# Performance work log

Hardware: AMD Instinct MI355X
Metric: run time of the kernel (lower is better)

The kernel has to match this reference:

```python
import jax, jax.numpy as jnp
import numpy as np

B, N, R = 4, 16, 64        # batch, permuted axis size, inner spatial size
M, S = N // 2, R * 2       # block count, block size


def _glorot(key, shape):
    fan_in, fan_out = shape[-2], shape[-1]
    lim = np.sqrt(6.0 / (fan_in + fan_out)).astype(np.float32)
    return jax.random.uniform(key, shape, jnp.float32, -lim, lim)


def setup_inputs() -> dict:
    key = jax.random.key(0)
    ks = jax.random.split(key, 10)
    inp = {
        "x": jax.random.normal(ks[0], (B, N, R, N, R, 2), jnp.float32),
        "perm_idx": jax.random.permutation(ks[1], N).astype(jnp.int32),
    }
    for i, name in enumerate(["hr1", "hi1", "hr2", "hi2", "hr3", "hi3", "hr4", "hi4"]):
        inp[name] = _glorot(ks[2 + i], (M, S, S))
    return inp


def _bilin(v, p_right, p_left):
    # v: (B, m, s, m, s). First contract the last s-axis against p_right's
    # block matmuls (block index = axis 3), then the axis-2 s-axis against
    # p_left's block matmuls (block index = axis 1).
    t = jnp.einsum('bmiaj,ajk->bmiak', v, p_right)
    return jnp.einsum('xbjci,bjk->xbkci', t, p_left)


def reference(x, perm_idx, hr1, hi1, hr2, hi2, hr3, hi3, hr4, hi4):
    m = x.shape[1] // 2
    s = x.shape[2] * 2
    n, r = m * 2, s // 2
    x = x.take(perm_idx, axis=1).take(perm_idx, axis=3)
    x = x.reshape((-1, m, s, m, s, 2))
    x_re, x_im = x[..., 0], x[..., 1]

    y_re = (_bilin(x_re, hr1, hr1) + _bilin(x_re, hi1, hi1)
            + _bilin(x_im, hi2, hr2) + _bilin(x_im, hr2, hi2))
    y_im = (_bilin(x_im, hr3, hr3) + _bilin(x_im, hi3, hi3)
            + _bilin(x_re, hi4, hr4) + _bilin(x_re, hr4, hi4))

    y = jnp.stack([y_re, y_im], axis=-1)
    return y.reshape((-1, n, r, n, r, 2))
```

## Files before the change

kernel.cpp:

```cpp
#include <hip/hip_runtime.h>
#include <hip/hip_bf16.h>
#include <stdint.h>

typedef __attribute__((ext_vector_type(8))) short bf16x8;
typedef __attribute__((ext_vector_type(4))) float f32x4;
typedef __attribute__((ext_vector_type(16))) float f32x16;

#define MFMA32(a, b, c) __builtin_amdgcn_mfma_f32_32x32x16_bf16((a), (b), (c), 0, 0, 0)

__device__ __forceinline__ unsigned short f2bf_rn(float f) {
    union { __bf16 b; unsigned short u; } v;
    v.b = (__bf16)f;
    return v.u;
}

__device__ __forceinline__ unsigned int pk2(float lo, float hi) {
    union { unsigned short s[2]; unsigned int u; } r;
    r.s[0] = f2bf_rn(lo); r.s[1] = f2bf_rn(hi);
    return r.u;
}

__device__ __forceinline__ void gload_lds16(const void* g, void* l) {
    __builtin_amdgcn_global_load_lds(
        (const __attribute__((address_space(1))) void*)g,
        (__attribute__((address_space(3))) void*)l, 16, 0, 0);
}

__global__ __launch_bounds__(256) void prep_h(
    const float* __restrict__ h0, const float* __restrict__ h1,
    const float* __restrict__ h2, const float* __restrict__ h3,
    const float* __restrict__ h4, const float* __restrict__ h5,
    const float* __restrict__ h6, const float* __restrict__ h7,
    unsigned short* __restrict__ ht)
{
    const float* hmap[8] = {h0, h1, h2, h3, h4, h5, h6, h7};
    const int wg = blockIdx.x;
    const int jblk = wg >> 2, qt = wg & 3;
    const float* src = hmap[jblk >> 3] + (jblk & 7) * 16384;
    unsigned short* dst = ht + jblk * 16384;
    __shared__ unsigned short tile[32 * 129];
    const int t = threadIdx.x;
    #pragma unroll
    for (int i = 0; i < 16; ++i) {
        int idx = t + 256 * i;
        int r = idx >> 5, kk = idx & 31;
        tile[kk * 129 + r] = f2bf_rn(src[r * 128 + qt * 32 + kk]);
    }
    __syncthreads();
    #pragma unroll
    for (int i = 0; i < 16; ++i) {
        int idx = t + 256 * i;
        int k = idx >> 7, r = idx & 127;
        dst[(qt * 32 + k) * 128 + r] = tile[k * 129 + r];
    }
}

__global__ __launch_bounds__(256, 1) void bilin_main(
    const float* __restrict__ x, const int* __restrict__ perm,
    const unsigned short* __restrict__ ht, float* __restrict__ out)
{
    const int wg = blockIdx.x;
    const int q = wg & 7, p = (wg >> 3) & 7, b = wg >> 6;
    const int tid = threadIdx.x;
    const int lane = tid & 63, wn = tid >> 6;
    const int l31 = lane & 31, hl = lane >> 5;

    __shared__ __align__(16) unsigned short smem[81920];
    unsigned short* xre_lds = smem;
    unsigned short* xim_lds = smem + 16384;
    unsigned short* llds = smem + 65536;

    constexpr int cseq[8]  = {0, 1, 6, 7, 2, 3, 4, 5};
    constexpr int rperm[8] = {0, 1, 3, 2, 4, 5, 7, 6};

    const int wubase = tid & ~63;
    auto stage_h = [&](unsigned short* dst, int blk) {
        const unsigned short* src = ht + blk * 16384;
        #pragma unroll
        for (int r = 0; r < 8; ++r) {
            const int idx = r * 256 + tid;
            const int row = idx >> 4, cin = idx & 15;
            gload_lds16(src + row * 128 + ((cin ^ (row & 15)) << 3),
                        dst + ((r * 256 + wubase) << 3));
        }
    };

    auto ldr = [&](const unsigned short* base, int row, int ch) -> bf16x8 {
        return *(const bf16x8*)(base + row * 128 + ((ch ^ (row & 15)) << 3));
    };

    auto stage_x_both = [&]() {
        #pragma unroll
        for (int i = 0; i < 8; ++i) {
            const int idx = i * 256 + tid;
            const int row = idx >> 4, cin = idx & 15;
            const int n1 = perm[2 * p + (row >> 6)];
            const int n2 = perm[2 * q + (cin >> 3)];
            const int r1 = row & 63, r2 = (cin & 7) * 8;
            const float* sp = x + ((size_t)((b * 16 + n1) * 64 + r1) * 1024
                                   + n2 * 64 + r2) * 2;
            float4 v0 = *(const float4*)(sp);
            float4 v1 = *(const float4*)(sp + 4);
            float4 v2 = *(const float4*)(sp + 8);
            float4 v3 = *(const float4*)(sp + 12);
            bf16x8 re, im;
            re[0] = (short)f2bf_rn(v0.x); re[1] = (short)f2bf_rn(v0.z);
            re[2] = (short)f2bf_rn(v1.x); re[3] = (short)f2bf_rn(v1.z);
            re[4] = (short)f2bf_rn(v2.x); re[5] = (short)f2bf_rn(v2.z);
            re[6] = (short)f2bf_rn(v3.x); re[7] = (short)f2bf_rn(v3.z);
            im[0] = (short)f2bf_rn(v0.y); im[1] = (short)f2bf_rn(v0.w);
            im[2] = (short)f2bf_rn(v1.y); im[3] = (short)f2bf_rn(v1.w);
            im[4] = (short)f2bf_rn(v2.y); im[5] = (short)f2bf_rn(v2.w);
            im[6] = (short)f2bf_rn(v3.y); im[7] = (short)f2bf_rn(v3.w);
            const int woff = row * 128 + ((cin ^ (row & 15)) << 3);
            *(bf16x8*)(xre_lds + woff) = re;
            *(bf16x8*)(xim_lds + woff) = im;
        }
    };

    bf16x8 xf[4][8];
    auto load_xf = [&](const unsigned short* plane) {
        #pragma unroll
        for (int m2 = 0; m2 < 4; ++m2)
            #pragma unroll
            for (int ks = 0; ks < 8; ++ks)
                xf[m2][ks] = ldr(plane, m2 * 32 + l31, 2 * ks + hl);
    };

    stage_h(smem + 32768, rperm[0] * 8 + q);
    stage_h(llds, 0 * 8 + p);
    stage_x_both();
    __syncthreads();
    load_xf(xre_lds);

    f32x16 yre[4], yim[4];
    #pragma unroll
    for (int i = 0; i < 4; ++i) {
        #pragma unroll
        for (int e = 0; e < 16; ++e) { yre[i][e] = 0.f; yim[i][e] = 0.f; }
    }

    #pragma unroll
    for (int cc = 0; cc < 8; ++cc) {
        const unsigned short* wb = smem + 32768 + (cc & 1) * 16384;

        if (cc < 7)
            stage_h(smem + 32768 + ((cc + 1) & 1) * 16384,
                    rperm[cseq[cc + 1]] * 8 + q);

        if (cc == 4) load_xf(xim_lds);

        f32x16 u[4];
        #pragma unroll
        for (int m2 = 0; m2 < 4; ++m2)
            #pragma unroll
            for (int e = 0; e < 16; ++e) u[m2][e] = 0.f;
        #pragma unroll
        for (int ks = 0; ks < 8; ++ks) {
            bf16x8 wfr = ldr(wb, wn * 32 + l31, 2 * ks + hl);
            #pragma unroll
            for (int m2 = 0; m2 < 4; ++m2)
                u[m2] = MFMA32(xf[m2][ks], wfr, u[m2]);
        }

        __syncthreads();

        #pragma unroll
        for (int t = 0; t < 8; ++t) {
            const int f = t >> 1, qa = (t & 1) * 2, qb = qa + 1;
            unsigned int lo0 = pk2(u[f][4 * qa + 0], u[f][4 * qa + 1]);
            unsigned int lo1 = pk2(u[f][4 * qa + 2], u[f][4 * qa + 3]);
            unsigned int hi0 = pk2(u[f][4 * qb + 0], u[f][4 * qb + 1]);
            unsigned int hi1 = pk2(u[f][4 * qb + 2], u[f][4 * qb + 3]);
            unsigned int send0 = hl ? lo0 : hi0;
            unsigned int send1 = hl ? lo1 : hi1;
            unsigned int sx0 = (unsigned int)__shfl_xor((int)send0, 32);
            unsigned int sx1 = (unsigned int)__shfl_xor((int)send1, 32);
            union { unsigned int d[4]; bf16x8 v; } ufu;
            ufu.d[0] = hl ? sx0 : lo0;
            ufu.d[1] = hl ? sx1 : lo1;
            ufu.d[2] = hl ? hi0 : sx0;
            ufu.d[3] = hl ? hi1 : sx1;
            #pragma unroll
            for (int mt = 0; mt < 4; ++mt) {
                bf16x8 lfr = ldr(llds, mt * 32 + l31, 2 * t + hl);
                if ((cc & 3) < 2) yre[mt] = MFMA32(lfr, ufu.v, yre[mt]);
                else              yim[mt] = MFMA32(lfr, ufu.v, yim[mt]);
            }
        }

        __syncthreads();
        if (cc < 7)
            stage_h(llds, cseq[cc + 1] * 8 + p);
    }

    float2* o2 = (float2*)out;
    #pragma unroll
    for (int mt = 0; mt < 4; ++mt)
        #pragma unroll
        for (int j = 0; j < 16; ++j) {
            const int row = mt * 32 + (j & 3) + 8 * (j >> 2) + 4 * hl;
            float2 v;
            v.x = yre[mt][j];
            v.y = yim[mt][j];
            o2[(size_t)(b * 1024 + p * 128 + row) * 1024
               + q * 128 + wn * 32 + l31] = v;
        }
}

extern "C" void kernel_launch(void* const* d_in, const int* in_sizes, int n_in,
                              void* d_out, int out_size, void* d_ws, size_t ws_size,
                              hipStream_t stream) {
    const float* x  = (const float*)d_in[0];
    const int* perm = (const int*)d_in[1];
    unsigned short* htp = (unsigned short*)d_ws;

    hipLaunchKernelGGL(prep_h, dim3(256), dim3(256), 0, stream,
        (const float*)d_in[2], (const float*)d_in[3], (const float*)d_in[4],
        (const float*)d_in[5], (const float*)d_in[6], (const float*)d_in[7],
        (const float*)d_in[8], (const float*)d_in[9], htp);
    hipLaunchKernelGGL(bilin_main, dim3(256), dim3(256), 0, stream,
        x, perm, htp, (float*)d_out);
}
```

Before: 39.48 us.

## Software-pipeline first and second block matmuls with double-buffered left weights

Restructures the main loop so the first-stage GEMM for the next chunk is interleaved with the second-stage GEMM of the current chunk. The right weights become triple-staged and the left weights double-buffered, which removes one barrier per iteration. Only one x plane is kept in LDS and it is restaged from global memory for the imaginary half. The goal is to hide LDS staging latency and keep the MFMA units busy, at the cost of higher register pressure and a second global read of x.

```diff
diff --git a/kernel.cpp b/kernel.cpp
--- a/kernel.cpp
+++ b/kernel.cpp
@@ -66,9 +66,7 @@
     const int l31 = lane & 31, hl = lane >> 5;
 
     __shared__ __align__(16) unsigned short smem[81920];
-    unsigned short* xre_lds = smem;
-    unsigned short* xim_lds = smem + 16384;
-    unsigned short* llds = smem + 65536;
+    unsigned short* xplane = smem;
 
     constexpr int cseq[8]  = {0, 1, 6, 7, 2, 3, 4, 5};
     constexpr int rperm[8] = {0, 1, 3, 2, 4, 5, 7, 6};
@@ -89,7 +87,7 @@
         return *(const bf16x8*)(base + row * 128 + ((ch ^ (row & 15)) << 3));
     };
 
-    auto stage_x_both = [&]() {
+    auto stage_x = [&](int g) {
         #pragma unroll
         for (int i = 0; i < 8; ++i) {
             const int idx = i * 256 + tid;
@@ -103,54 +101,47 @@
             float4 v1 = *(const float4*)(sp + 4);
             float4 v2 = *(const float4*)(sp + 8);
             float4 v3 = *(const float4*)(sp + 12);
-            bf16x8 re, im;
-            re[0] = (short)f2bf_rn(v0.x); re[1] = (short)f2bf_rn(v0.z);
-            re[2] = (short)f2bf_rn(v1.x); re[3] = (short)f2bf_rn(v1.z);
-            re[4] = (short)f2bf_rn(v2.x); re[5] = (short)f2bf_rn(v2.z);
-            re[6] = (short)f2bf_rn(v3.x); re[7] = (short)f2bf_rn(v3.z);
-            im[0] = (short)f2bf_rn(v0.y); im[1] = (short)f2bf_rn(v0.w);
-            im[2] = (short)f2bf_rn(v1.y); im[3] = (short)f2bf_rn(v1.w);
-            im[4] = (short)f2bf_rn(v2.y); im[5] = (short)f2bf_rn(v2.w);
-            im[6] = (short)f2bf_rn(v3.y); im[7] = (short)f2bf_rn(v3.w);
-            const int woff = row * 128 + ((cin ^ (row & 15)) << 3);
-            *(bf16x8*)(xre_lds + woff) = re;
-            *(bf16x8*)(xim_lds + woff) = im;
+            bf16x8 t;
+            if (g == 0) {
+                t[0] = (short)f2bf_rn(v0.x); t[1] = (short)f2bf_rn(v0.z);
+                t[2] = (short)f2bf_rn(v1.x); t[3] = (short)f2bf_rn(v1.z);
+                t[4] = (short)f2bf_rn(v2.x); t[5] = (short)f2bf_rn(v2.z);
+                t[6] = (short)f2bf_rn(v3.x); t[7] = (short)f2bf_rn(v3.z);
+            } else {
+                t[0] = (short)f2bf_rn(v0.y); t[1] = (short)f2bf_rn(v0.w);
+                t[2] = (short)f2bf_rn(v1.y); t[3] = (short)f2bf_rn(v1.w);
+                t[4] = (short)f2bf_rn(v2.y); t[5] = (short)f2bf_rn(v2.w);
+                t[6] = (short)f2bf_rn(v3.y); t[7] = (short)f2bf_rn(v3.w);
+            }
+            *(bf16x8*)(xplane + row * 128 + ((cin ^ (row & 15)) << 3)) = t;
         }
     };
 
     bf16x8 xf[4][8];
-    auto load_xf = [&](const unsigned short* plane) {
+    auto load_xf = [&]() {
         #pragma unroll
         for (int m2 = 0; m2 < 4; ++m2)
             #pragma unroll
             for (int ks = 0; ks < 8; ++ks)
-                xf[m2][ks] = ldr(plane, m2 * 32 + l31, 2 * ks + hl);
-    };
-
-    stage_h(smem + 32768, rperm[0] * 8 + q);
-    stage_h(llds, 0 * 8 + p);
-    stage_x_both();
+                xf[m2][ks] = ldr(xplane, m2 * 32 + l31, 2 * ks + hl);
+    };
+
+    stage_h(smem + 16384, rperm[cseq[0]] * 8 + q);
+    stage_h(smem + 32768, rperm[cseq[1]] * 8 + q);
+    stage_h(smem + 49152, cseq[0] * 8 + p);
+    stage_x(0);
     __syncthreads();
-    load_xf(xre_lds);
-
-    f32x16 yre[4], yim[4];
-    #pragma unroll
-    for (int i = 0; i < 4; ++i) {
+    load_xf();
+    __syncthreads();
+
+    f32x16 yre[4], yim[4], u[4];
+    #pragma unroll
+    for (int i = 0; i < 4; ++i)
         #pragma unroll
         for (int e = 0; e < 16; ++e) { yre[i][e] = 0.f; yim[i][e] = 0.f; }
-    }
-
-    #pragma unroll
-    for (int cc = 0; cc < 8; ++cc) {
-        const unsigned short* wb = smem + 32768 + (cc & 1) * 16384;
-
-        if (cc < 7)
-            stage_h(smem + 32768 + ((cc + 1) & 1) * 16384,
-                    rperm[cseq[cc + 1]] * 8 + q);
-
-        if (cc == 4) load_xf(xim_lds);
-
-        f32x16 u[4];
+
+    {
+        const unsigned short* wb = smem + 16384;
         #pragma unroll
         for (int m2 = 0; m2 < 4; ++m2)
             #pragma unroll
@@ -162,36 +153,82 @@
             for (int m2 = 0; m2 < 4; ++m2)
                 u[m2] = MFMA32(xf[m2][ks], wfr, u[m2]);
         }
-
+    }
+    stage_x(1);
+
+    auto BT = [&](int t, const unsigned short* lb, bool isRe) {
+        const int f = t >> 1, qa = (t & 1) * 2, qb = qa + 1;
+        unsigned int lo0 = pk2(u[f][4 * qa + 0], u[f][4 * qa + 1]);
+        unsigned int lo1 = pk2(u[f][4 * qa + 2], u[f][4 * qa + 3]);
+        unsigned int hi0 = pk2(u[f][4 * qb + 0], u[f][4 * qb + 1]);
+        unsigned int hi1 = pk2(u[f][4 * qb + 2], u[f][4 * qb + 3]);
+        unsigned int send0 = hl ? lo0 : hi0;
+        unsigned int send1 = hl ? lo1 : hi1;
+        unsigned int sx0 = (unsigned int)__shfl_xor((int)send0, 32);
+        unsigned int sx1 = (unsigned int)__shfl_xor((int)send1, 32);
+        union { unsigned int d[4]; bf16x8 v; } ufu;
+        ufu.d[0] = hl ? sx0 : lo0;
+        ufu.d[1] = hl ? sx1 : lo1;
+        ufu.d[2] = hl ? hi0 : sx0;
+        ufu.d[3] = hl ? hi1 : sx1;
+        #pragma unroll
+        for (int mt = 0; mt < 4; ++mt) {
+            bf16x8 lfr = ldr(lb, mt * 32 + l31, 2 * t + hl);
+            if (isRe) yre[mt] = MFMA32(lfr, ufu.v, yre[mt]);
+            else      yim[mt] = MFMA32(lfr, ufu.v, yim[mt]);
+        }
+    };
+
+    #pragma unroll
+    for (int cc = 0; cc < 8; ++cc) {
         __syncthreads();
 
-        #pragma unroll
-        for (int t = 0; t < 8; ++t) {
-            const int f = t >> 1, qa = (t & 1) * 2, qb = qa + 1;
-            unsigned int lo0 = pk2(u[f][4 * qa + 0], u[f][4 * qa + 1]);
-            unsigned int lo1 = pk2(u[f][4 * qa + 2], u[f][4 * qa + 3]);
-            unsigned int hi0 = pk2(u[f][4 * qb + 0], u[f][4 * qb + 1]);
-            unsigned int hi1 = pk2(u[f][4 * qb + 2], u[f][4 * qb + 3]);
-            unsigned int send0 = hl ? lo0 : hi0;
-            unsigned int send1 = hl ? lo1 : hi1;
-            unsigned int sx0 = (unsigned int)__shfl_xor((int)send0, 32);
-            unsigned int sx1 = (unsigned int)__shfl_xor((int)send1, 32);
-            union { unsigned int d[4]; bf16x8 v; } ufu;
-            ufu.d[0] = hl ? sx0 : lo0;
-            ufu.d[1] = hl ? sx1 : lo1;
-            ufu.d[2] = hl ? hi0 : sx0;
-            ufu.d[3] = hl ? hi1 : sx1;
-            #pragma unroll
-            for (int mt = 0; mt < 4; ++mt) {
-                bf16x8 lfr = ldr(llds, mt * 32 + l31, 2 * t + hl);
-                if ((cc & 3) < 2) yre[mt] = MFMA32(lfr, ufu.v, yre[mt]);
-                else              yim[mt] = MFMA32(lfr, ufu.v, yim[mt]);
+        if (cc < 6)
+            stage_h(smem + 16384 + (cc & 1) * 16384,
+                    rperm[cseq[cc + 2]] * 8 + q);
+        if (cc < 7)
+            stage_h(smem + 49152 + ((cc + 1) & 1) * 16384,
+                    cseq[cc + 1] * 8 + p);
+
+        if (cc == 3) load_xf();
+
+        const unsigned short* lb  = smem + 49152 + (cc & 1) * 16384;
+        const unsigned short* wbn = smem + 16384 + ((cc + 1) & 1) * 16384;
+        const bool isRe = (cc & 3) < 2;
+
+        bf16x8 wfc[8];
+        if (cc < 7) {
+            #pragma unroll
+            for (int ks = 0; ks < 8; ++ks)
+                wfc[ks] = ldr(wbn, wn * 32 + l31, 2 * ks + hl);
+        }
+
+        BT(0, lb, isRe); BT(1, lb, isRe); BT(2, lb, isRe); BT(3, lb, isRe);
+        if (cc < 7) {
+            #pragma unroll
+            for (int m2 = 0; m2 < 2; ++m2) {
+                f32x16 acc;
+                #pragma unroll
+                for (int e = 0; e < 16; ++e) acc[e] = 0.f;
+                #pragma unroll
+                for (int ks = 0; ks < 8; ++ks)
+                    acc = MFMA32(xf[m2][ks], wfc[ks], acc);
+                u[m2] = acc;
             }
         }
-
-        __syncthreads();
-        if (cc < 7)
-            stage_h(llds, cseq[cc + 1] * 8 + p);
+        BT(4, lb, isRe); BT(5, lb, isRe); BT(6, lb, isRe); BT(7, lb, isRe);
+        if (cc < 7) {
+            #pragma unroll
+            for (int m2 = 2; m2 < 4; ++m2) {
+                f32x16 acc;
+                #pragma unroll
+                for (int e = 0; e < 16; ++e) acc[e] = 0.f;
+                #pragma unroll
+                for (int ks = 0; ks < 8; ++ks)
+                    acc = MFMA32(xf[m2][ks], wfc[ks], acc);
+                u[m2] = acc;
+            }
+        }
     }
 
     float2* o2 = (float2*)out;
```

After: 50.92 us. 1.29x slower.
